# Optimization experiments

Hardware: AMD Instinct MI355X
Metric: run time of the kernel (lower is better)

Reference implementation:

```python
import jax, jax.numpy as jnp
import numpy as np

DIM = 2048
NUM_GATES = 8
TOP_N = 2
EPS = 1e-9
B, N = 2, 4096
CAPACITY_FACTOR = 1.25  # train
MIN_EXPERT_CAPACITY = 4
THRESHOLD = np.array([EPS, 0.2], dtype=np.float32)  # [eps, *threshold_train]


def setup_inputs() -> dict:
    key = jax.random.key(0)
    kx, kw, kp = jax.random.split(key, 3)
    x = jax.random.normal(kx, (B, N, DIM), jnp.float32)
    W = jax.random.normal(kw, (NUM_GATES, DIM), jnp.float32) * 0.02  # Linear(dim, num_gates, bias=False)
    probs = jax.random.uniform(kp, (TOP_N, B, N), jnp.float32)       # the uniform draw inside forward
    return {"x": x, "W": W, "probs": probs}


def reference(x, W, probs):
    b, n, d = x.shape
    cap = max(min(n, int(n * CAPACITY_FACTOR / NUM_GATES)), MIN_EXPERT_CAPACITY)
    dt = x.dtype

    gate_logits = jnp.einsum('bnd,ed->bne', x, W)            # [b,n,e]
    raw_gates = jax.nn.softmax(gate_logits, axis=-1)
    gates, gate_idx = jax.lax.top_k(raw_gates, TOP_N)        # [b,n,k]
    gates = jnp.moveaxis(gates, -1, 0)                       # [k,b,n]
    gate_idx = jnp.moveaxis(gate_idx, -1, 0)                 # [k,b,n]
    one_hot_e = jax.nn.one_hot(gate_idx, NUM_GATES, dtype=dt)  # [k,b,n,e]

    denom = jnp.clip(gates.sum(0, keepdims=True), EPS, None)
    gates = gates / denom                                    # renormalized top-n gates

    thr = jnp.clip(jnp.asarray(THRESHOLD, dt), EPS, None)[:, None, None]
    should_route = probs < gates / thr                       # [k,b,n]
    should_route = should_route.at[0].set(True)              # top-1 always routes
    mask = one_hot_e * should_route[..., None].astype(dt)    # [k,b,n,e]

    # exclusive cumsum over the sequence dim (position of each token in its expert queue)
    mask_cumsum = jnp.cumsum(mask, axis=2) - mask            # [k,b,n,e]

    combine = jnp.zeros((b, n, NUM_GATES, cap), dt)
    prev_expert_count = jnp.zeros((b, 1, NUM_GATES), dt)
    final_masks = []
    for k in range(TOP_N):  # tiny fixed loop over top-n slots
        pos = (mask_cumsum[k] + prev_expert_count) * mask[k]          # [b,n,e]
        mk = mask[k] * (pos < float(cap)).astype(dt)                  # drop over-capacity tokens
        prev_expert_count = prev_expert_count + mk.sum(axis=1, keepdims=True)
        pos_flat = pos.sum(axis=-1)                                   # [b,n]
        mflat = mk.sum(axis=-1)                                       # [b,n] in {0,1}
        pos_oh = jax.nn.one_hot(pos_flat.astype(jnp.int32), cap, dtype=dt)  # out-of-range -> zeros (safe_one_hot)
        # gates_k * mask_flat * one_hot_e * pos_one_hot; mflat^2 == mflat, one_hot_e*mflat == mk
        combine = combine + jnp.einsum('bn,bne,bnc->bnec', gates[k] * mflat, mk, pos_oh)
        final_masks.append(mk)

    dispatch = (combine != 0).astype(dt)
    # straight-through dispatch tensor
    dispatch = dispatch + combine - jax.lax.stop_gradient(combine)

    # training losses (mask[0] was mutated in-place in torch -> use final capacity-clipped top-1 mask)
    density_1 = final_masks[0].mean(axis=1)                  # [b,e]
    density_1_proxy = raw_gates.mean(axis=1)                 # [b,e]
    balance_loss = (density_1_proxy * density_1).mean() * float(NUM_GATES ** 2)
    router_z_loss = jnp.mean(jnp.square(jax.nn.logsumexp(gate_logits, axis=-1)))

    return dispatch, combine, balance_loss, router_z_loss
```

## Files before the change

### kernel.cpp

```cpp
#include <hip/hip_runtime.h>


#define DIMX 2048
#define NG   8
#define NB   2
#define NSEQ 4096
#define NTOK (NB*NSEQ)
#define CAPE 640
#define ROW  (NG*CAPE)
#define DCNT ((size_t)NTOK*ROW)

struct Ws {
  int   pk[NTOK];
  float g0[NTOK];
  float g1[NTOK];
  float z2[NTOK];
  float raws[(size_t)NTOK*NG];
  int   pos0[NTOK];
  int   pos1[NTOK];
  float proxy[16];
  int   cnt0[16];
};

__global__ __launch_bounds__(512) void kgate(const float* __restrict__ x,
                                             const float* __restrict__ W,
                                             const float* __restrict__ probs,
                                             Ws* __restrict__ ws) {
  __shared__ float4 Wl[NG * 512];
  int tid = threadIdx.x;
  for (int i = tid; i < NG * 512; i += 512) Wl[i] = ((const float4*)W)[i];
  __syncthreads();

  int wave = tid >> 6, lane = tid & 63;
  int token = blockIdx.x * 8 + wave;

  const float4* xp = (const float4*)(x + (size_t)token * DIMX);
  float4 xv[8];
#pragma unroll
  for (int j = 0; j < 8; ++j) xv[j] = xp[j * 64 + lane];

  float acc[NG] = {0.f,0.f,0.f,0.f,0.f,0.f,0.f,0.f};
#pragma unroll
  for (int j = 0; j < 8; ++j) {
    float4 xj = xv[j];
#pragma unroll
    for (int e = 0; e < NG; ++e) {
      float4 w = Wl[e * 512 + j * 64 + lane];
      acc[e] = fmaf(xj.x, w.x, acc[e]);
      acc[e] = fmaf(xj.y, w.y, acc[e]);
      acc[e] = fmaf(xj.z, w.z, acc[e]);
      acc[e] = fmaf(xj.w, w.w, acc[e]);
    }
  }
#pragma unroll
  for (int e = 0; e < NG; ++e) {
#pragma unroll
    for (int off = 32; off > 0; off >>= 1) acc[e] += __shfl_xor(acc[e], off, 64);
  }

  float m = acc[0];
#pragma unroll
  for (int e = 1; e < NG; ++e) m = fmaxf(m, acc[e]);
  float ex[NG], s = 0.f;
#pragma unroll
  for (int e = 0; e < NG; ++e) { ex[e] = expf(acc[e] - m); s += ex[e]; }
  float raw[NG];
#pragma unroll
  for (int e = 0; e < NG; ++e) raw[e] = ex[e] / s;

  int e0i = 0; float g0v = raw[0];
#pragma unroll
  for (int e = 1; e < NG; ++e) if (raw[e] > g0v) { g0v = raw[e]; e0i = e; }
  int e1i = -1; float g1v = -1.f;
#pragma unroll
  for (int e = 0; e < NG; ++e) if (e != e0i && raw[e] > g1v) { g1v = raw[e]; e1i = e; }

  float denom = g0v + g1v;
  if (denom < 1e-9f) denom = 1e-9f;
  float g0n = g0v / denom, g1n = g1v / denom;

  int b = token >> 12, n = token & (NSEQ - 1);
  float p1 = probs[NB * NSEQ + b * NSEQ + n];
  int r = (p1 < (g1n / 0.2f)) ? 1 : 0;

  float lse = m + logf(s);

  if (lane < NG) ws->raws[(size_t)token * NG + lane] = raw[lane];
  if (lane == 0) {
    ws->pk[token] = e0i | (e1i << 4) | (r << 8);
    ws->g0[token] = g0n;  ws->g1[token] = g1n;
    ws->z2[token] = lse * lse;
  }
}

__global__ __launch_bounds__(256) void kscan(Ws* __restrict__ ws) {
  __shared__ int   wtot[4];
  __shared__ float wsum[4];
  int be = blockIdx.x, b = be >> 3, e = be & 7;
  int t = threadIdx.x, wave = t >> 6, lane = t & 63;
  int base = b * NSEQ;

  int pk[16];
  {
    const int4* pp = (const int4*)(ws->pk + base + t * 16);
#pragma unroll
    for (int j = 0; j < 4; ++j) {
      int4 v = pp[j];
      pk[4*j] = v.x; pk[4*j+1] = v.y; pk[4*j+2] = v.z; pk[4*j+3] = v.w;
    }
  }

  float ps = 0.f;
#pragma unroll
  for (int i = 0; i < 16; ++i) ps += ws->raws[(size_t)(base + t * 16 + i) * NG + e];
#pragma unroll
  for (int off = 32; off > 0; off >>= 1) ps += __shfl_xor(ps, off, 64);
  if (lane == 0) wsum[wave] = ps;

  int cnt = 0;
#pragma unroll
  for (int i = 0; i < 16; ++i) cnt += ((pk[i] & 15) == e);
  int incl = cnt;
#pragma unroll
  for (int off = 1; off < 64; off <<= 1) { int v = __shfl_up(incl, off, 64); if (lane >= off) incl += v; }
  if (lane == 63) wtot[wave] = incl;
  __syncthreads();
  int woff = 0, tot = 0;
#pragma unroll
  for (int w = 0; w < 4; ++w) { int v = wtot[w]; tot += v; if (w < wave) woff += v; }
  int c0 = min(tot, CAPE);
  int p = woff + incl - cnt;
#pragma unroll
  for (int i = 0; i < 16; ++i) {
    if ((pk[i] & 15) == e) { ws->pos0[base + t * 16 + i] = (p < CAPE) ? p : -1; ++p; }
  }
  __syncthreads();

  cnt = 0;
#pragma unroll
  for (int i = 0; i < 16; ++i) cnt += ((((pk[i] >> 4) & 15) == e) && (pk[i] & 0x100));
  incl = cnt;
#pragma unroll
  for (int off = 1; off < 64; off <<= 1) { int v = __shfl_up(incl, off, 64); if (lane >= off) incl += v; }
  if (lane == 63) wtot[wave] = incl;
  __syncthreads();
  woff = 0;
#pragma unroll
  for (int w = 0; w < 4; ++w) { int v = wtot[w]; if (w < wave) woff += v; }
  p = woff + incl - cnt;
#pragma unroll
  for (int i = 0; i < 16; ++i) {
    if (((pk[i] >> 4) & 15) == e) {
      if (pk[i] & 0x100) { int q = p + c0; ws->pos1[base + t * 16 + i] = (q < CAPE) ? q : -1; ++p; }
      else               { ws->pos1[base + t * 16 + i] = -1; }
    }
  }

  if (t == 0) {
    ws->proxy[be] = wsum[0] + wsum[1] + wsum[2] + wsum[3];
    ws->cnt0[be]  = c0;
  }
}

__global__ __launch_bounds__(256) void kout(const Ws* __restrict__ ws, float* __restrict__ out) {
  int token = blockIdx.x;
  int t = threadIdx.x;
  int pkv = ws->pk[token];
  int e0 = pkv & 15, e1 = (pkv >> 4) & 15;
  int p0 = ws->pos0[token], p1 = ws->pos1[token];
  float g0 = ws->g0[token], g1 = ws->g1[token];
  int o0 = (p0 >= 0) ? e0 * CAPE + p0 : -16;
  int o1 = (p1 >= 0) ? e1 * CAPE + p1 : -16;

  float* drow = out + (size_t)token * ROW;
  float* crow = out + DCNT + (size_t)token * ROW;

#pragma unroll
  for (int c = 0; c < 5; ++c) {
    int off = c * 1024 + t * 4;
    int r0 = o0 - off, r1 = o1 - off;
    float4 dv, cv;
    dv.x = ((r0 == 0) | (r1 == 0)) ? 1.f : 0.f;
    dv.y = ((r0 == 1) | (r1 == 1)) ? 1.f : 0.f;
    dv.z = ((r0 == 2) | (r1 == 2)) ? 1.f : 0.f;
    dv.w = ((r0 == 3) | (r1 == 3)) ? 1.f : 0.f;
    cv.x = (r0 == 0) ? g0 : ((r1 == 0) ? g1 : 0.f);
    cv.y = (r0 == 1) ? g0 : ((r1 == 1) ? g1 : 0.f);
    cv.z = (r0 == 2) ? g0 : ((r1 == 2) ? g1 : 0.f);
    cv.w = (r0 == 3) ? g0 : ((r1 == 3) ? g1 : 0.f);
    *(float4*)(drow + off) = dv;
    *(float4*)(crow + off) = cv;
  }

  if (token == 0) {
    __shared__ float red[256];
    float s = 0.f;
    const float4* zz = (const float4*)ws->z2;
    for (int i = t; i < NTOK / 4; i += 256) { float4 v = zz[i]; s += v.x + v.y + v.z + v.w; }
    red[t] = s; __syncthreads();
    for (int st = 128; st > 0; st >>= 1) { if (t < st) red[t] += red[t + st]; __syncthreads(); }
    if (t == 0) {
      float bal = 0.f;
      for (int i = 0; i < 16; ++i)
        bal += (ws->proxy[i] * (1.f / NSEQ)) * ((float)ws->cnt0[i] * (1.f / NSEQ));
      out[2 * DCNT]     = bal * (64.f / 16.f);
      out[2 * DCNT + 1] = red[0] / (float)NTOK;
    }
  }
}

extern "C" void kernel_launch(void* const* d_in, const int* in_sizes, int n_in,
                              void* d_out, int out_size, void* d_ws, size_t ws_size,
                              hipStream_t stream) {
  const float* x     = (const float*)d_in[0];
  const float* W     = (const float*)d_in[1];
  const float* probs = (const float*)d_in[2];
  float* out = (float*)d_out;
  Ws* ws = (Ws*)d_ws;

  kgate<<<NTOK / 8, 512, 0, stream>>>(x, W, probs, ws);
  kscan<<<16, 256, 0, stream>>>(ws);
  kout<<<NTOK, 256, 0, stream>>>(ws, out);
}
```

Measured before the change: 93.23 us.

## Fuse output zero-fill into gate kernel and scatter nonzeros from scan

The gate kernel now also zero-fills the dispatch and combine tensors with a grid-stride loop, split before and after the gate compute by block parity, so the fill overlaps the x reads. The scan kernel writes the few nonzero dispatch and combine entries directly at their computed positions. This removes the dense per-token output kernel and the pos workspace arrays. The risk is that the scattered writes are serialized across only 16 blocks.

```diff
diff --git a/kernel.cpp b/kernel.cpp
--- a/kernel.cpp
+++ b/kernel.cpp
@@ -16,16 +16,15 @@
   float g1[NTOK];
   float z2[NTOK];
   float raws[(size_t)NTOK*NG];
-  int   pos0[NTOK];
-  int   pos1[NTOK];
   float proxy[16];
   int   cnt0[16];
 };
 
-__global__ __launch_bounds__(512) void kgate(const float* __restrict__ x,
+__global__ __launch_bounds__(512) void kmain(const float* __restrict__ x,
                                              const float* __restrict__ W,
                                              const float* __restrict__ probs,
-                                             Ws* __restrict__ ws) {
+                                             Ws* __restrict__ ws,
+                                             float4* __restrict__ out4) {
   __shared__ float4 Wl[NG * 512];
   int tid = threadIdx.x;
   for (int i = tid; i < NG * 512; i += 512) Wl[i] = ((const float4*)W)[i];
@@ -34,66 +33,83 @@
   int wave = tid >> 6, lane = tid & 63;
   int token = blockIdx.x * 8 + wave;
 
-  const float4* xp = (const float4*)(x + (size_t)token * DIMX);
-  float4 xv[8];
-#pragma unroll
-  for (int j = 0; j < 8; ++j) xv[j] = xp[j * 64 + lane];
-
-  float acc[NG] = {0.f,0.f,0.f,0.f,0.f,0.f,0.f,0.f};
-#pragma unroll
-  for (int j = 0; j < 8; ++j) {
-    float4 xj = xv[j];
+  const long n4 = (long)(2 * DCNT) / 4;
+  const long zbase = (long)blockIdx.x * 512 + tid;
+  const long zstr  = 512L * (NTOK / 8);
+  const float4 zv = make_float4(0.f, 0.f, 0.f, 0.f);
+
+  if (blockIdx.x & 1) {
+    for (long i = zbase; i < n4; i += zstr) out4[i] = zv;
+  }
+
+  {
+    const float4* xp = (const float4*)(x + (size_t)token * DIMX);
+    float4 xv[8];
+#pragma unroll
+    for (int j = 0; j < 8; ++j) xv[j] = xp[j * 64 + lane];
+
+    float acc[NG] = {0.f,0.f,0.f,0.f,0.f,0.f,0.f,0.f};
+#pragma unroll
+    for (int j = 0; j < 8; ++j) {
+      float4 xj = xv[j];
+#pragma unroll
+      for (int e = 0; e < NG; ++e) {
+        float4 w = Wl[e * 512 + j * 64 + lane];
+        acc[e] = fmaf(xj.x, w.x, acc[e]);
+        acc[e] = fmaf(xj.y, w.y, acc[e]);
+        acc[e] = fmaf(xj.z, w.z, acc[e]);
+        acc[e] = fmaf(xj.w, w.w, acc[e]);
+      }
+    }
 #pragma unroll
     for (int e = 0; e < NG; ++e) {
-      float4 w = Wl[e * 512 + j * 64 + lane];
-      acc[e] = fmaf(xj.x, w.x, acc[e]);
-      acc[e] = fmaf(xj.y, w.y, acc[e]);
-      acc[e] = fmaf(xj.z, w.z, acc[e]);
-      acc[e] = fmaf(xj.w, w.w, acc[e]);
-    }
-  }
-#pragma unroll
-  for (int e = 0; e < NG; ++e) {
-#pragma unroll
-    for (int off = 32; off > 0; off >>= 1) acc[e] += __shfl_xor(acc[e], off, 64);
-  }
-
-  float m = acc[0];
-#pragma unroll
-  for (int e = 1; e < NG; ++e) m = fmaxf(m, acc[e]);
-  float ex[NG], s = 0.f;
-#pragma unroll
-  for (int e = 0; e < NG; ++e) { ex[e] = expf(acc[e] - m); s += ex[e]; }
-  float raw[NG];
-#pragma unroll
-  for (int e = 0; e < NG; ++e) raw[e] = ex[e] / s;
-
-  int e0i = 0; float g0v = raw[0];
-#pragma unroll
-  for (int e = 1; e < NG; ++e) if (raw[e] > g0v) { g0v = raw[e]; e0i = e; }
-  int e1i = -1; float g1v = -1.f;
-#pragma unroll
-  for (int e = 0; e < NG; ++e) if (e != e0i && raw[e] > g1v) { g1v = raw[e]; e1i = e; }
-
-  float denom = g0v + g1v;
-  if (denom < 1e-9f) denom = 1e-9f;
-  float g0n = g0v / denom, g1n = g1v / denom;
-
-  int b = token >> 12, n = token & (NSEQ - 1);
-  float p1 = probs[NB * NSEQ + b * NSEQ + n];
-  int r = (p1 < (g1n / 0.2f)) ? 1 : 0;
-
-  float lse = m + logf(s);
-
-  if (lane < NG) ws->raws[(size_t)token * NG + lane] = raw[lane];
-  if (lane == 0) {
-    ws->pk[token] = e0i | (e1i << 4) | (r << 8);
-    ws->g0[token] = g0n;  ws->g1[token] = g1n;
-    ws->z2[token] = lse * lse;
-  }
-}
-
-__global__ __launch_bounds__(256) void kscan(Ws* __restrict__ ws) {
+#pragma unroll
+      for (int off = 32; off > 0; off >>= 1) acc[e] += __shfl_xor(acc[e], off, 64);
+    }
+
+    float m = acc[0];
+#pragma unroll
+    for (int e = 1; e < NG; ++e) m = fmaxf(m, acc[e]);
+    float ex[NG], s = 0.f;
+#pragma unroll
+    for (int e = 0; e < NG; ++e) { ex[e] = expf(acc[e] - m); s += ex[e]; }
+    float raw[NG];
+#pragma unroll
+    for (int e = 0; e < NG; ++e) raw[e] = ex[e] / s;
+
+    int e0i = 0; float g0v = raw[0];
+#pragma unroll
+    for (int e = 1; e < NG; ++e) if (raw[e] > g0v) { g0v = raw[e]; e0i = e; }
+    int e1i = -1; float g1v = -1.f;
+#pragma unroll
+    for (int e = 0; e < NG; ++e) if (e != e0i && raw[e] > g1v) { g1v = raw[e]; e1i = e; }
+
+    float denom = g0v + g1v;
+    if (denom < 1e-9f) denom = 1e-9f;
+    float g0n = g0v / denom, g1n = g1v / denom;
+
+    int b = token >> 12, n = token & (NSEQ - 1);
+    float p1 = probs[NB * NSEQ + b * NSEQ + n];
+    int r = (p1 < (g1n / 0.2f)) ? 1 : 0;
+
+    float lse = m + logf(s);
+
+    if (lane < NG) ws->raws[(size_t)token * NG + lane] = raw[lane];
+    if (lane == 0) {
+      ws->pk[token] = e0i | (e1i << 4) | (r << 8);
+      ws->g0[token] = g0n;  ws->g1[token] = g1n;
+      ws->z2[token] = lse * lse;
+    }
+  }
+
+  if (!(blockIdx.x & 1)) {
+    for (long i = zbase; i < n4; i += zstr) out4[i] = zv;
+  }
+}
+
+__global__ __launch_bounds__(256) void kscan(const Ws* __restrict__ wsc,
+                                             Ws* __restrict__ ws,
+                                             float* __restrict__ out) {
   __shared__ int   wtot[4];
   __shared__ float wsum[4];
   int be = blockIdx.x, b = be >> 3, e = be & 7;
@@ -102,7 +118,7 @@
 
   int pk[16];
   {
-    const int4* pp = (const int4*)(ws->pk + base + t * 16);
+    const int4* pp = (const int4*)(wsc->pk + base + t * 16);
 #pragma unroll
     for (int j = 0; j < 4; ++j) {
       int4 v = pp[j];
@@ -112,7 +128,7 @@
 
   float ps = 0.f;
 #pragma unroll
-  for (int i = 0; i < 16; ++i) ps += ws->raws[(size_t)(base + t * 16 + i) * NG + e];
+  for (int i = 0; i < 16; ++i) ps += wsc->raws[(size_t)(base + t * 16 + i) * NG + e];
 #pragma unroll
   for (int off = 32; off > 0; off >>= 1) ps += __shfl_xor(ps, off, 64);
   if (lane == 0) wsum[wave] = ps;
@@ -132,7 +148,15 @@
   int p = woff + incl - cnt;
 #pragma unroll
   for (int i = 0; i < 16; ++i) {
-    if ((pk[i] & 15) == e) { ws->pos0[base + t * 16 + i] = (p < CAPE) ? p : -1; ++p; }
+    int nn = t * 16 + i;
+    if ((pk[i] & 15) == e) {
+      if (p < CAPE) {
+        size_t o = (size_t)(base + nn) * ROW + e * CAPE + p;
+        out[o]        = 1.f;
+        out[DCNT + o] = wsc->g0[base + nn];
+      }
+      ++p;
+    }
   }
   __syncthreads();
 
@@ -150,9 +174,15 @@
   p = woff + incl - cnt;
 #pragma unroll
   for (int i = 0; i < 16; ++i) {
-    if (((pk[i] >> 4) & 15) == e) {
-      if (pk[i] & 0x100) { int q = p + c0; ws->pos1[base + t * 16 + i] = (q < CAPE) ? q : -1; ++p; }
-      else               { ws->pos1[base + t * 16 + i] = -1; }
+    int nn = t * 16 + i;
+    if ((((pk[i] >> 4) & 15) == e) && (pk[i] & 0x100)) {
+      int q = p + c0;
+      if (q < CAPE) {
+        size_t o = (size_t)(base + nn) * ROW + e * CAPE + q;
+        out[o]        = 1.f;
+        out[DCNT + o] = wsc->g1[base + nn];
+      }
+      ++p;
     }
   }
 
@@ -162,50 +192,20 @@
   }
 }
 
-__global__ __launch_bounds__(256) void kout(const Ws* __restrict__ ws, float* __restrict__ out) {
-  int token = blockIdx.x;
+__global__ __launch_bounds__(256) void kloss(const Ws* __restrict__ ws, float* __restrict__ outs) {
+  __shared__ float red[256];
   int t = threadIdx.x;
-  int pkv = ws->pk[token];
-  int e0 = pkv & 15, e1 = (pkv >> 4) & 15;
-  int p0 = ws->pos0[token], p1 = ws->pos1[token];
-  float g0 = ws->g0[token], g1 = ws->g1[token];
-  int o0 = (p0 >= 0) ? e0 * CAPE + p0 : -16;
-  int o1 = (p1 >= 0) ? e1 * CAPE + p1 : -16;
-
-  float* drow = out + (size_t)token * ROW;
-  float* crow = out + DCNT + (size_t)token * ROW;
-
-#pragma unroll
-  for (int c = 0; c < 5; ++c) {
-    int off = c * 1024 + t * 4;
-    int r0 = o0 - off, r1 = o1 - off;
-    float4 dv, cv;
-    dv.x = ((r0 == 0) | (r1 == 0)) ? 1.f : 0.f;
-    dv.y = ((r0 == 1) | (r1 == 1)) ? 1.f : 0.f;
-    dv.z = ((r0 == 2) | (r1 == 2)) ? 1.f : 0.f;
-    dv.w = ((r0 == 3) | (r1 == 3)) ? 1.f : 0.f;
-    cv.x = (r0 == 0) ? g0 : ((r1 == 0) ? g1 : 0.f);
-    cv.y = (r0 == 1) ? g0 : ((r1 == 1) ? g1 : 0.f);
-    cv.z = (r0 == 2) ? g0 : ((r1 == 2) ? g1 : 0.f);
-    cv.w = (r0 == 3) ? g0 : ((r1 == 3) ? g1 : 0.f);
-    *(float4*)(drow + off) = dv;
-    *(float4*)(crow + off) = cv;
-  }
-
-  if (token == 0) {
-    __shared__ float red[256];
-    float s = 0.f;
-    const float4* zz = (const float4*)ws->z2;
-    for (int i = t; i < NTOK / 4; i += 256) { float4 v = zz[i]; s += v.x + v.y + v.z + v.w; }
-    red[t] = s; __syncthreads();
-    for (int st = 128; st > 0; st >>= 1) { if (t < st) red[t] += red[t + st]; __syncthreads(); }
-    if (t == 0) {
-      float bal = 0.f;
-      for (int i = 0; i < 16; ++i)
-        bal += (ws->proxy[i] * (1.f / NSEQ)) * ((float)ws->cnt0[i] * (1.f / NSEQ));
-      out[2 * DCNT]     = bal * (64.f / 16.f);
-      out[2 * DCNT + 1] = red[0] / (float)NTOK;
-    }
+  float s = 0.f;
+  const float4* zz = (const float4*)ws->z2;
+  for (int i = t; i < NTOK / 4; i += 256) { float4 v = zz[i]; s += v.x + v.y + v.z + v.w; }
+  red[t] = s; __syncthreads();
+  for (int st = 128; st > 0; st >>= 1) { if (t < st) red[t] += red[t + st]; __syncthreads(); }
+  if (t == 0) {
+    float bal = 0.f;
+    for (int i = 0; i < 16; ++i)
+      bal += (ws->proxy[i] * (1.f / NSEQ)) * ((float)ws->cnt0[i] * (1.f / NSEQ));
+    outs[0] = bal * (64.f / 16.f);
+    outs[1] = red[0] / (float)NTOK;
   }
 }
 
@@ -218,7 +218,7 @@
   float* out = (float*)d_out;
   Ws* ws = (Ws*)d_ws;
 
-  kgate<<<NTOK / 8, 512, 0, stream>>>(x, W, probs, ws);
-  kscan<<<16, 256, 0, stream>>>(ws);
-  kout<<<NTOK, 256, 0, stream>>>(ws, out);
-}
+  kmain<<<NTOK / 8, 512, 0, stream>>>(x, W, probs, ws, (float4*)out);
+  kscan<<<16, 256, 0, stream>>>(ws, ws, out);
+  kloss<<<1, 256, 0, stream>>>(ws, out + 2 * DCNT);
+}
```

After: 111.8 us. +19.9%, slower.

## Process four tokens per wave in gate kernel and fold loss reductions into scan

Applied to the files above, without the earlier changes.

The gate kernel now assigns four tokens to each wave, so every LDS load of W is reused across four tokens, and the grid shrinks to a quarter of the blocks. Raw softmax gates are stored transposed (expert-major), which makes the per-expert proxy sums in the scan kernel contiguous reads. The z-loss and balance-loss reductions move out of the serial token-0 tail of the output kernel into the scan blocks, which combine them with atomics after a memset. In exchange the gate kernel needs more registers and has fewer blocks in flight, and the float atomics make the summation order nondeterministic.

```diff
diff --git a/kernel.cpp b/kernel.cpp
--- a/kernel.cpp
+++ b/kernel.cpp
@@ -15,87 +15,113 @@
   float g0[NTOK];
   float g1[NTOK];
   float z2[NTOK];
-  float raws[(size_t)NTOK*NG];
   int   pos0[NTOK];
   int   pos1[NTOK];
-  float proxy[16];
-  int   cnt0[16];
+  float raws_t[NG][NTOK];
 };
 
-__global__ __launch_bounds__(512) void kgate(const float* __restrict__ x,
-                                             const float* __restrict__ W,
-                                             const float* __restrict__ probs,
-                                             Ws* __restrict__ ws) {
+__global__ __launch_bounds__(512, 4) void kgate(const float* __restrict__ x,
+                                                const float* __restrict__ W,
+                                                const float* __restrict__ probs,
+                                                Ws* __restrict__ ws) {
   __shared__ float4 Wl[NG * 512];
   int tid = threadIdx.x;
   for (int i = tid; i < NG * 512; i += 512) Wl[i] = ((const float4*)W)[i];
   __syncthreads();
 
   int wave = tid >> 6, lane = tid & 63;
-  int token = blockIdx.x * 8 + wave;
-
-  const float4* xp = (const float4*)(x + (size_t)token * DIMX);
-  float4 xv[8];
-#pragma unroll
-  for (int j = 0; j < 8; ++j) xv[j] = xp[j * 64 + lane];
-
-  float acc[NG] = {0.f,0.f,0.f,0.f,0.f,0.f,0.f,0.f};
+  int t0 = blockIdx.x * 32 + wave * 4;
+
+  const float4* xp0 = (const float4*)(x + (size_t)(t0 + 0) * DIMX);
+  const float4* xp1 = (const float4*)(x + (size_t)(t0 + 1) * DIMX);
+  const float4* xp2 = (const float4*)(x + (size_t)(t0 + 2) * DIMX);
+  const float4* xp3 = (const float4*)(x + (size_t)(t0 + 3) * DIMX);
+
+  float acc[4][NG];
+#pragma unroll
+  for (int tk = 0; tk < 4; ++tk)
+#pragma unroll
+    for (int e = 0; e < NG; ++e) acc[tk][e] = 0.f;
+
 #pragma unroll
   for (int j = 0; j < 8; ++j) {
-    float4 xj = xv[j];
+    float4 x0 = xp0[j * 64 + lane];
+    float4 x1 = xp1[j * 64 + lane];
+    float4 x2 = xp2[j * 64 + lane];
+    float4 x3 = xp3[j * 64 + lane];
 #pragma unroll
     for (int e = 0; e < NG; ++e) {
       float4 w = Wl[e * 512 + j * 64 + lane];
-      acc[e] = fmaf(xj.x, w.x, acc[e]);
-      acc[e] = fmaf(xj.y, w.y, acc[e]);
-      acc[e] = fmaf(xj.z, w.z, acc[e]);
-      acc[e] = fmaf(xj.w, w.w, acc[e]);
-    }
-  }
-#pragma unroll
-  for (int e = 0; e < NG; ++e) {
-#pragma unroll
-    for (int off = 32; off > 0; off >>= 1) acc[e] += __shfl_xor(acc[e], off, 64);
-  }
-
-  float m = acc[0];
-#pragma unroll
-  for (int e = 1; e < NG; ++e) m = fmaxf(m, acc[e]);
-  float ex[NG], s = 0.f;
-#pragma unroll
-  for (int e = 0; e < NG; ++e) { ex[e] = expf(acc[e] - m); s += ex[e]; }
-  float raw[NG];
-#pragma unroll
-  for (int e = 0; e < NG; ++e) raw[e] = ex[e] / s;
-
-  int e0i = 0; float g0v = raw[0];
-#pragma unroll
-  for (int e = 1; e < NG; ++e) if (raw[e] > g0v) { g0v = raw[e]; e0i = e; }
-  int e1i = -1; float g1v = -1.f;
-#pragma unroll
-  for (int e = 0; e < NG; ++e) if (e != e0i && raw[e] > g1v) { g1v = raw[e]; e1i = e; }
-
-  float denom = g0v + g1v;
-  if (denom < 1e-9f) denom = 1e-9f;
-  float g0n = g0v / denom, g1n = g1v / denom;
-
-  int b = token >> 12, n = token & (NSEQ - 1);
-  float p1 = probs[NB * NSEQ + b * NSEQ + n];
-  int r = (p1 < (g1n / 0.2f)) ? 1 : 0;
-
-  float lse = m + logf(s);
-
-  if (lane < NG) ws->raws[(size_t)token * NG + lane] = raw[lane];
-  if (lane == 0) {
-    ws->pk[token] = e0i | (e1i << 4) | (r << 8);
-    ws->g0[token] = g0n;  ws->g1[token] = g1n;
-    ws->z2[token] = lse * lse;
-  }
-}
-
-__global__ __launch_bounds__(256) void kscan(Ws* __restrict__ ws) {
+      acc[0][e] = fmaf(x0.x, w.x, acc[0][e]);
+      acc[0][e] = fmaf(x0.y, w.y, acc[0][e]);
+      acc[0][e] = fmaf(x0.z, w.z, acc[0][e]);
+      acc[0][e] = fmaf(x0.w, w.w, acc[0][e]);
+      acc[1][e] = fmaf(x1.x, w.x, acc[1][e]);
+      acc[1][e] = fmaf(x1.y, w.y, acc[1][e]);
+      acc[1][e] = fmaf(x1.z, w.z, acc[1][e]);
+      acc[1][e] = fmaf(x1.w, w.w, acc[1][e]);
+      acc[2][e] = fmaf(x2.x, w.x, acc[2][e]);
+      acc[2][e] = fmaf(x2.y, w.y, acc[2][e]);
+      acc[2][e] = fmaf(x2.z, w.z, acc[2][e]);
+      acc[2][e] = fmaf(x2.w, w.w, acc[2][e]);
+      acc[3][e] = fmaf(x3.x, w.x, acc[3][e]);
+      acc[3][e] = fmaf(x3.y, w.y, acc[3][e]);
+      acc[3][e] = fmaf(x3.z, w.z, acc[3][e]);
+      acc[3][e] = fmaf(x3.w, w.w, acc[3][e]);
+    }
+  }
+
+#pragma unroll
+  for (int tk = 0; tk < 4; ++tk) {
+    int token = t0 + tk;
+    float a[NG];
+#pragma unroll
+    for (int e = 0; e < NG; ++e) a[e] = acc[tk][e];
+#pragma unroll
+    for (int e = 0; e < NG; ++e) {
+#pragma unroll
+      for (int off = 32; off > 0; off >>= 1) a[e] += __shfl_xor(a[e], off, 64);
+    }
+
+    float m = a[0];
+#pragma unroll
+    for (int e = 1; e < NG; ++e) m = fmaxf(m, a[e]);
+    float ex[NG], s = 0.f;
+#pragma unroll
+    for (int e = 0; e < NG; ++e) { ex[e] = expf(a[e] - m); s += ex[e]; }
+    float raw[NG];
+#pragma unroll
+    for (int e = 0; e < NG; ++e) raw[e] = ex[e] / s;
+
+    int e0i = 0; float g0v = raw[0];
+#pragma unroll
+    for (int e = 1; e < NG; ++e) if (raw[e] > g0v) { g0v = raw[e]; e0i = e; }
+    int e1i = -1; float g1v = -1.f;
+#pragma unroll
+    for (int e = 0; e < NG; ++e) if (e != e0i && raw[e] > g1v) { g1v = raw[e]; e1i = e; }
+
+    float denom = g0v + g1v;
+    if (denom < 1e-9f) denom = 1e-9f;
+    float g0n = g0v / denom, g1n = g1v / denom;
+
+    float p1 = probs[NTOK + token];
+    int r = (p1 < (g1n / 0.2f)) ? 1 : 0;
+
+    float lse = m + logf(s);
+
+    if (lane < NG) ws->raws_t[lane][token] = raw[lane];
+    if (lane == 0) {
+      ws->pk[token] = e0i | (e1i << 4) | (r << 8);
+      ws->g0[token] = g0n;  ws->g1[token] = g1n;
+      ws->z2[token] = lse * lse;
+    }
+  }
+}
+
+__global__ __launch_bounds__(256) void kscan(Ws* __restrict__ ws, float* __restrict__ losses) {
   __shared__ int   wtot[4];
   __shared__ float wsum[4];
+  __shared__ float zsum[4];
   int be = blockIdx.x, b = be >> 3, e = be & 7;
   int t = threadIdx.x, wave = t >> 6, lane = t & 63;
   int base = b * NSEQ;
@@ -111,11 +137,23 @@
   }
 
   float ps = 0.f;
-#pragma unroll
-  for (int i = 0; i < 16; ++i) ps += ws->raws[(size_t)(base + t * 16 + i) * NG + e];
+  {
+    const float* rp = ws->raws_t[e] + base + t * 16;
+#pragma unroll
+    for (int i = 0; i < 16; ++i) ps += rp[i];
+  }
 #pragma unroll
   for (int off = 32; off > 0; off >>= 1) ps += __shfl_xor(ps, off, 64);
   if (lane == 0) wsum[wave] = ps;
+
+  float zs = 0.f;
+  if (t < 128) {
+    float4 v = ((const float4*)ws->z2)[be * 128 + t];
+    zs = v.x + v.y + v.z + v.w;
+  }
+#pragma unroll
+  for (int off = 32; off > 0; off >>= 1) zs += __shfl_xor(zs, off, 64);
+  if (lane == 0) zsum[wave] = zs;
 
   int cnt = 0;
 #pragma unroll
@@ -150,15 +188,17 @@
   p = woff + incl - cnt;
 #pragma unroll
   for (int i = 0; i < 16; ++i) {
-    if (((pk[i] >> 4) & 15) == e) {
+    if ((((pk[i] >> 4) & 15) == e)) {
       if (pk[i] & 0x100) { int q = p + c0; ws->pos1[base + t * 16 + i] = (q < CAPE) ? q : -1; ++p; }
       else               { ws->pos1[base + t * 16 + i] = -1; }
     }
   }
 
   if (t == 0) {
-    ws->proxy[be] = wsum[0] + wsum[1] + wsum[2] + wsum[3];
-    ws->cnt0[be]  = c0;
+    float psum = wsum[0] + wsum[1] + wsum[2] + wsum[3];
+    float ztot = zsum[0] + zsum[1] + zsum[2] + zsum[3];
+    atomicAdd(losses + 0, psum * (1.f / NSEQ) * ((float)c0 * (1.f / NSEQ)) * 4.f);
+    atomicAdd(losses + 1, ztot * (1.f / NTOK));
   }
 }
 
@@ -191,22 +231,6 @@
     *(float4*)(drow + off) = dv;
     *(float4*)(crow + off) = cv;
   }
-
-  if (token == 0) {
-    __shared__ float red[256];
-    float s = 0.f;
-    const float4* zz = (const float4*)ws->z2;
-    for (int i = t; i < NTOK / 4; i += 256) { float4 v = zz[i]; s += v.x + v.y + v.z + v.w; }
-    red[t] = s; __syncthreads();
-    for (int st = 128; st > 0; st >>= 1) { if (t < st) red[t] += red[t + st]; __syncthreads(); }
-    if (t == 0) {
-      float bal = 0.f;
-      for (int i = 0; i < 16; ++i)
-        bal += (ws->proxy[i] * (1.f / NSEQ)) * ((float)ws->cnt0[i] * (1.f / NSEQ));
-      out[2 * DCNT]     = bal * (64.f / 16.f);
-      out[2 * DCNT + 1] = red[0] / (float)NTOK;
-    }
-  }
 }
 
 extern "C" void kernel_launch(void* const* d_in, const int* in_sizes, int n_in,
@@ -218,7 +242,8 @@
   float* out = (float*)d_out;
   Ws* ws = (Ws*)d_ws;
 
-  kgate<<<NTOK / 8, 512, 0, stream>>>(x, W, probs, ws);
-  kscan<<<16, 256, 0, stream>>>(ws);
+  hipMemsetAsync(out + 2 * DCNT, 0, 2 * sizeof(float), stream);
+  kgate<<<NTOK / 32, 512, 0, stream>>>(x, W, probs, ws);
+  kscan<<<16, 256, 0, stream>>>(ws, out + 2 * DCNT);
   kout<<<NTOK, 256, 0, stream>>>(ws, out);
 }
```

Measured after the change: 214.3 us. 2.3x slower.
